# Kernel optimization log

Measured on AMD Instinct MI355X. Metric: run time of the kernel, lower is better.

## Reference

```python
import jax, jax.numpy as jnp
import numpy as np

TOP_K = 2


def setup_inputs() -> dict:
    key = jax.random.key(0)
    ks = jax.random.split(key, 4)
    T, E, D_IN, D_H, D_OUT = 8192, 8, 1024, 4096, 1024
    s_in = 1.0 / np.sqrt(D_IN)
    s_h = 1.0 / np.sqrt(D_H)
    return {
        "x": jax.random.normal(ks[0], (T, D_IN), dtype=jnp.float32),
        "Wg": jax.random.normal(ks[1], (D_IN, E), dtype=jnp.float32) * s_in,
        "bg": jnp.zeros((E,), dtype=jnp.float32),
        "W1": jax.random.normal(ks[2], (E, D_IN, D_H), dtype=jnp.float32) * s_in,
        "b1": jnp.zeros((E, D_H), dtype=jnp.float32),
        "W2": jax.random.normal(ks[3], (E, D_H, D_OUT), dtype=jnp.float32) * s_h,
        "b2": jnp.zeros((E, D_OUT), dtype=jnp.float32),
    }


def moe_forward(x, Wg, bg, W1, b1, W2, b2):
    # Top-k gate: logits [T,E] -> top-k -> softmax over the k selected logits,
    # scattered back into a dense [T,E] weight matrix (zeros elsewhere).
    logits = x @ Wg + bg                              # [T, E]
    topv, topi = jax.lax.top_k(logits, TOP_K)         # [T, k]
    topw = jax.nn.softmax(topv, axis=-1)              # [T, k]
    T, E = logits.shape
    weights = jnp.zeros((T, E), dtype=logits.dtype)
    rows = jnp.arange(T)[:, None]
    weights = weights.at[rows, topi].set(topw)        # dense gate weights [T, E]

    # Dense all-expert MLP (faithful to the naive torch module):
    h = jax.nn.relu(jnp.einsum("ti,eih->teh", x, W1) + b1[None])   # [T, E, H]
    expert_out = jnp.einsum("teh,eho->teo", h, W2) + b2[None]      # [T, E, O]

    # Top-k weighted sum over experts.
    return jnp.einsum("te,teo->to", weights, expert_out)           # [T, O]


def reference(x, Wg, bg, W1, b1, W2, b2):
    return moe_forward(x, Wg, bg, W1, b1, W2, b2)
```

## Files before the change

kernel.cpp:

```cpp
#include <hip/hip_runtime.h>
#include <hip/hip_bf16.h>
#include <stdint.h>

#define NTOK 8192
#define NE 8
#define DIN 1024
#define DH 4096
#define DOUT 1024
#define MAXMB 135

typedef __bf16 bf16;
typedef __bf16 bf16_8 __attribute__((ext_vector_type(8)));
typedef __bf16 bf16_4 __attribute__((ext_vector_type(4)));
typedef float f32_4 __attribute__((ext_vector_type(4)));

__device__ __forceinline__ void gl_lds16(const void* g, void* l) {
  __builtin_amdgcn_global_load_lds(
      (const __attribute__((address_space(1))) unsigned int*)g,
      (__attribute__((address_space(3))) unsigned int*)l, 16, 0, 0);
}

__global__ void gate_kernel(const float* __restrict__ x, const float* __restrict__ Wg,
                            const float* __restrict__ bg,
                            int* __restrict__ topi, float* __restrict__ topw) {
  int t = blockIdx.x * 4 + (threadIdx.x >> 6);
  int lane = threadIdx.x & 63;
  float acc[NE];
#pragma unroll
  for (int e = 0; e < NE; e++) acc[e] = 0.f;
  const float* xr = x + (size_t)t * DIN;
#pragma unroll
  for (int i = 0; i < DIN / 64; i++) {
    float xv = xr[lane + 64 * i];
    const float4* wr = (const float4*)(Wg + (size_t)(lane + 64 * i) * NE);
    float4 w0 = wr[0], w1 = wr[1];
    acc[0] += xv * w0.x; acc[1] += xv * w0.y; acc[2] += xv * w0.z; acc[3] += xv * w0.w;
    acc[4] += xv * w1.x; acc[5] += xv * w1.y; acc[6] += xv * w1.z; acc[7] += xv * w1.w;
  }
#pragma unroll
  for (int off = 32; off > 0; off >>= 1)
#pragma unroll
    for (int e = 0; e < NE; e++) acc[e] += __shfl_xor(acc[e], off, 64);
  if (lane == 0) {
    float lg[NE];
#pragma unroll
    for (int e = 0; e < NE; e++) lg[e] = acc[e] + bg[e];
    int i0 = 0; float v0 = lg[0];
#pragma unroll
    for (int e = 1; e < NE; e++) if (lg[e] > v0) { v0 = lg[e]; i0 = e; }
    int i1 = -1; float v1 = -3.0e38f;
#pragma unroll
    for (int e = 0; e < NE; e++) if (e != i0 && lg[e] > v1) { v1 = lg[e]; i1 = e; }
    float ex = expf(v1 - v0);
    float w0 = 1.f / (1.f + ex);
    float w1 = ex / (1.f + ex);
    topi[2 * t] = i0; topi[2 * t + 1] = i1;
    topw[2 * t] = w0; topw[2 * t + 1] = w1;
  }
}

__global__ void hist_kernel(const int* __restrict__ topi, int* __restrict__ counts,
                            int* __restrict__ pos) {
  __shared__ int bins[NE];
  __shared__ int base[NE];
  int tid = threadIdx.x;
  if (tid < NE) bins[tid] = 0;
  __syncthreads();
  int i = blockIdx.x * 256 + tid;
  int e = topi[i];
  int local = atomicAdd(&bins[e], 1);
  __syncthreads();
  if (tid < NE) base[tid] = atomicAdd(&counts[tid], bins[tid]);
  __syncthreads();
  pos[i] = base[e] + local;
}

__global__ void scan_kernel(const int* counts, int* offsets, int* mblk_off) {
  if (threadIdx.x == 0) {
    int s = 0, b = 0;
    for (int e = 0; e < NE; e++) {
      offsets[e] = s; mblk_off[e] = b;
      s += counts[e]; b += (counts[e] + 127) >> 7;
    }
    mblk_off[NE] = b;
  }
}

__global__ void pack_kernel(const int* __restrict__ topi,
                            const int* __restrict__ pos, const int* __restrict__ offsets,
                            int* __restrict__ tok_list, int* __restrict__ slot_of) {
  int i = blockIdx.x * 256 + threadIdx.x;
  int e = topi[i];
  int slot = offsets[e] + pos[i];
  tok_list[slot] = i >> 1;
  slot_of[i] = slot;
}

__global__ void cvtx_kernel(const float* __restrict__ x, bf16* __restrict__ xb) {
  size_t i = ((size_t)blockIdx.x * 256 + threadIdx.x) * 8;
  float4 a = *(const float4*)(x + i);
  float4 b = *(const float4*)(x + i + 4);
  bf16_8 o;
  o[0] = (bf16)a.x; o[1] = (bf16)a.y; o[2] = (bf16)a.z; o[3] = (bf16)a.w;
  o[4] = (bf16)b.x; o[5] = (bf16)b.y; o[6] = (bf16)b.z; o[7] = (bf16)b.w;
  *(bf16_8*)(xb + i) = o;
}

__global__ void tcvt_kernel(const float* __restrict__ src, bf16* __restrict__ dst,
                            int src_ld, long long src_es, int dst_ld, long long dst_es) {
  __shared__ bf16 tile[32][33];
  const float* s = src + blockIdx.z * src_es + (size_t)(blockIdx.x * 32) * src_ld + blockIdx.y * 32;
  bf16* d = dst + blockIdx.z * dst_es + (size_t)(blockIdx.y * 32) * dst_ld + blockIdx.x * 32;
  int tid = threadIdx.x;
  int r = tid >> 3, c4 = (tid & 7) * 4;
  float4 v = *(const float4*)(s + (size_t)r * src_ld + c4);
  tile[r][c4] = (bf16)v.x; tile[r][c4 + 1] = (bf16)v.y;
  tile[r][c4 + 2] = (bf16)v.z; tile[r][c4 + 3] = (bf16)v.w;
  __syncthreads();
  int n = tid >> 3, k4 = (tid & 7) * 4;
  bf16_4 o;
  o[0] = tile[k4][n]; o[1] = tile[k4 + 1][n]; o[2] = tile[k4 + 2][n]; o[3] = tile[k4 + 3][n];
  *(bf16_4*)(d + (size_t)n * dst_ld + k4) = o;
}


__global__ __launch_bounds__(256) void gemm1_kernel(
    const bf16* __restrict__ xb, const bf16* __restrict__ W1t,
    const float* __restrict__ b1, const int* __restrict__ counts,
    const int* __restrict__ offsets, const int* __restrict__ mblk_off,
    const int* __restrict__ tok_list,
    bf16* __restrict__ h, int hchunk, int hc0) {
  int mb = blockIdx.y;
  if (mb >= mblk_off[NE]) return;
  int e = 0;
  while (mb >= mblk_off[e + 1]) e++;
  int ne = counts[e];
  int m0 = (mb - mblk_off[e]) * 128;
  int off = offsets[e];
  int n0 = blockIdx.x * 128;

  __shared__ bf16 ldsA[128 * 32];
  __shared__ bf16 ldsB[128 * 32];

  int tid = threadIdx.x;
  int w = tid >> 6, lane = tid & 63;
  int scol = (((lane & 3) ^ (lane >> 3)) & 3) * 8;

  const bf16* gA[2]; const bf16* gB[2];
  bf16* lA[2]; bf16* lB[2];
#pragma unroll
  for (int j = 0; j < 2; j++) {
    int seg = w * 2 + j;
    int row = seg * 16 + (lane >> 2);
    int slot = off + m0 + row;
    int smax = off + ne - 1;
    if (slot > smax) slot = smax;
    int tok = tok_list[slot];
    gA[j] = xb + (size_t)tok * DIN + scol;
    lA[j] = ldsA + seg * 512;
    gB[j] = W1t + ((size_t)e * hchunk + n0 + row) * DIN + scol;
    lB[j] = ldsB + seg * 512;
  }

  f32_4 acc[4][4];
#pragma unroll
  for (int i = 0; i < 4; i++)
#pragma unroll
    for (int j = 0; j < 4; j++) acc[i][j] = (f32_4){0.f, 0.f, 0.f, 0.f};

  int wm = w & 1, wn = w >> 1;
  int lr = lane & 15, quad = lane >> 4;
  int rcol = ((quad ^ (lr >> 1)) & 3) * 8;

  for (int kt = 0; kt < DIN / 32; kt++) {
#pragma unroll
    for (int j = 0; j < 2; j++) {
      gl_lds16(gA[j], lA[j]);
      gl_lds16(gB[j], lB[j]);
    }
    gA[0] += 32; gA[1] += 32; gB[0] += 32; gB[1] += 32;
    __syncthreads();
    bf16_8 af[4], bfr[4];
#pragma unroll
    for (int mt = 0; mt < 4; mt++)
      af[mt] = *(const bf16_8*)(ldsA + (wm * 64 + mt * 16 + lr) * 32 + rcol);
#pragma unroll
    for (int nt = 0; nt < 4; nt++)
      bfr[nt] = *(const bf16_8*)(ldsB + (wn * 64 + nt * 16 + lr) * 32 + rcol);
#pragma unroll
    for (int mt = 0; mt < 4; mt++)
#pragma unroll
      for (int nt = 0; nt < 4; nt++)
        acc[mt][nt] = __builtin_amdgcn_mfma_f32_16x16x32_bf16(af[mt], bfr[nt], acc[mt][nt], 0, 0, 0);
    __syncthreads();
  }

#pragma unroll
  for (int nt = 0; nt < 4; nt++) {
    int cloc = wn * 64 + nt * 16 + lr;
    int c = n0 + cloc;
    float bias = b1[(size_t)e * DH + hc0 + c];
#pragma unroll
    for (int mt = 0; mt < 4; mt++) {
#pragma unroll
      for (int r2 = 0; r2 < 4; r2++) {
        int row = wm * 64 + mt * 16 + quad * 4 + r2;
        if (m0 + row < ne) {
          float v = acc[mt][nt][r2] + bias;
          v = v > 0.f ? v : 0.f;
          h[(size_t)(off + m0 + row) * hchunk + c] = (bf16)v;
        }
      }
    }
  }
}

__global__ __launch_bounds__(256) void gemm2_kernel(
    const bf16* __restrict__ h, const bf16* __restrict__ W2t,
    const int* __restrict__ counts, const int* __restrict__ offsets,
    const int* __restrict__ mblk_off,
    float* __restrict__ y, int hchunk, int accum) {
  int mb = blockIdx.y;
  if (mb >= mblk_off[NE]) return;
  int e = 0;
  while (mb >= mblk_off[e + 1]) e++;
  int ne = counts[e];
  int m0 = (mb - mblk_off[e]) * 128;
  int off = offsets[e];
  int n0 = blockIdx.x * 128;

  __shared__ bf16 ldsA[128 * 32];
  __shared__ bf16 ldsB[128 * 32];

  int tid = threadIdx.x;
  int w = tid >> 6, lane = tid & 63;
  int scol = (((lane & 3) ^ (lane >> 3)) & 3) * 8;

  const bf16* gA[2]; const bf16* gB[2];
  bf16* lA[2]; bf16* lB[2];
#pragma unroll
  for (int j = 0; j < 2; j++) {
    int seg = w * 2 + j;
    int row = seg * 16 + (lane >> 2);
    gA[j] = h + (size_t)(off + m0 + row) * hchunk + scol;
    lA[j] = ldsA + seg * 512;
    gB[j] = W2t + ((size_t)e * DOUT + n0 + row) * hchunk + scol;
    lB[j] = ldsB + seg * 512;
  }

  f32_4 acc[4][4];
#pragma unroll
  for (int i = 0; i < 4; i++)
#pragma unroll
    for (int j = 0; j < 4; j++) acc[i][j] = (f32_4){0.f, 0.f, 0.f, 0.f};

  int wm = w & 1, wn = w >> 1;
  int lr = lane & 15, quad = lane >> 4;
  int rcol = ((quad ^ (lr >> 1)) & 3) * 8;

  for (int kt = 0; kt < hchunk / 32; kt++) {
#pragma unroll
    for (int j = 0; j < 2; j++) {
      gl_lds16(gA[j], lA[j]);
      gl_lds16(gB[j], lB[j]);
    }
    gA[0] += 32; gA[1] += 32; gB[0] += 32; gB[1] += 32;
    __syncthreads();
    bf16_8 af[4], bfr[4];
#pragma unroll
    for (int mt = 0; mt < 4; mt++)
      af[mt] = *(const bf16_8*)(ldsA + (wm * 64 + mt * 16 + lr) * 32 + rcol);
#pragma unroll
    for (int nt = 0; nt < 4; nt++)
      bfr[nt] = *(const bf16_8*)(ldsB + (wn * 64 + nt * 16 + lr) * 32 + rcol);
#pragma unroll
    for (int mt = 0; mt < 4; mt++)
#pragma unroll
      for (int nt = 0; nt < 4; nt++)
        acc[mt][nt] = __builtin_amdgcn_mfma_f32_16x16x32_bf16(af[mt], bfr[nt], acc[mt][nt], 0, 0, 0);
    __syncthreads();
  }

#pragma unroll
  for (int mt = 0; mt < 4; mt++) {
#pragma unroll
    for (int r2 = 0; r2 < 4; r2++) {
      int row = wm * 64 + mt * 16 + quad * 4 + r2;
      if (m0 + row < ne) {
        float* yrow = y + (size_t)(off + m0 + row) * DOUT + n0;
#pragma unroll
        for (int nt = 0; nt < 4; nt++) {
          int c = wn * 64 + nt * 16 + lr;
          float v = acc[mt][nt][r2];
          if (accum) v += yrow[c];
          yrow[c] = v;
        }
      }
    }
  }
}

__global__ void combine_kernel(const int* __restrict__ topi, const float* __restrict__ topw,
                               const int* __restrict__ slot_of, const float* __restrict__ y,
                               const float* __restrict__ b2, float* __restrict__ out) {
  int t = blockIdx.x;
  int c = threadIdx.x * 4;
  int e0 = topi[2 * t], e1 = topi[2 * t + 1];
  float w0 = topw[2 * t], w1 = topw[2 * t + 1];
  int s0 = slot_of[2 * t], s1 = slot_of[2 * t + 1];
  float4 a = *(const float4*)(y + (size_t)s0 * DOUT + c);
  float4 b = *(const float4*)(y + (size_t)s1 * DOUT + c);
  float4 p = *(const float4*)(b2 + (size_t)e0 * DOUT + c);
  float4 q = *(const float4*)(b2 + (size_t)e1 * DOUT + c);
  float4 o;
  o.x = w0 * (a.x + p.x) + w1 * (b.x + q.x);
  o.y = w0 * (a.y + p.y) + w1 * (b.y + q.y);
  o.z = w0 * (a.z + p.z) + w1 * (b.z + q.z);
  o.w = w0 * (a.w + p.w) + w1 * (b.w + q.w);
  *(float4*)(out + (size_t)t * DOUT + c) = o;
}

extern "C" void kernel_launch(void* const* d_in, const int* in_sizes, int n_in,
                              void* d_out, int out_size, void* d_ws, size_t ws_size,
                              hipStream_t stream) {
  const float* x  = (const float*)d_in[0];
  const float* Wg = (const float*)d_in[1];
  const float* bg = (const float*)d_in[2];
  const float* W1 = (const float*)d_in[3];
  const float* b1 = (const float*)d_in[4];
  const float* W2 = (const float*)d_in[5];
  const float* b2 = (const float*)d_in[6];
  float* out = (float*)d_out;

  char* p = (char*)d_ws;
  int*   counts   = (int*)p;   p += 256;
  int*   offsets  = (int*)p;   p += 256;
  int*   mblk_off = (int*)p;   p += 256;
  int*   topi     = (int*)p;   p += 16384 * 4;
  float* topw     = (float*)p; p += 16384 * 4;
  int*   pos      = (int*)p;   p += 16384 * 4;
  int*   tok_list = (int*)p;   p += 16384 * 4;
  int*   slot_of  = (int*)p;   p += 16384 * 4;
  bf16*  xb       = (bf16*)p;  p += (size_t)NTOK * DIN * 2;
  float* y        = (float*)p; p += (size_t)16384 * DOUT * 4;

  size_t fixedBytes = (size_t)(p - (char*)d_ws);
  int hchunk = 4096;
  while (hchunk > 128 && fixedBytes + (size_t)hchunk * 65792 > ws_size) hchunk >>= 1;

  bf16* W1t  = (bf16*)p; p += (size_t)NE * hchunk * DIN * 2;
  bf16* W2t  = (bf16*)p; p += (size_t)NE * DOUT * hchunk * 2;
  bf16* hbuf = (bf16*)p; p += (size_t)(16384 + 128) * hchunk * 2;

  hipMemsetAsync(counts, 0, 32, stream);
  gate_kernel<<<NTOK / 4, 256, 0, stream>>>(x, Wg, bg, topi, topw);
  cvtx_kernel<<<(NTOK * DIN) / (8 * 256), 256, 0, stream>>>(x, xb);
  hist_kernel<<<64, 256, 0, stream>>>(topi, counts, pos);
  scan_kernel<<<1, 64, 0, stream>>>(counts, offsets, mblk_off);
  pack_kernel<<<64, 256, 0, stream>>>(topi, pos, offsets, tok_list, slot_of);

  int nchunks = DH / hchunk;
  for (int c = 0; c < nchunks; c++) {
    int hc0 = c * hchunk;
    tcvt_kernel<<<dim3(DIN / 32, hchunk / 32, NE), 256, 0, stream>>>(
        W1 + hc0, W1t, DH, (long long)DIN * DH, DIN, (long long)hchunk * DIN);
    tcvt_kernel<<<dim3(hchunk / 32, DOUT / 32, NE), 256, 0, stream>>>(
        W2 + (size_t)hc0 * DOUT, W2t, DOUT, (long long)DH * DOUT, hchunk, (long long)DOUT * hchunk);
    gemm1_kernel<<<dim3(hchunk / 128, MAXMB), 256, 0, stream>>>(
        xb, W1t, b1, counts, offsets, mblk_off, tok_list, hbuf, hchunk, hc0);
    gemm2_kernel<<<dim3(DOUT / 128, MAXMB), 256, 0, stream>>>(
        hbuf, W2t, counts, offsets, mblk_off, y, hchunk, c > 0 ? 1 : 0);
  }
  combine_kernel<<<NTOK, 256, 0, stream>>>(topi, topw, slot_of, y, b2, out);
}
```

Baseline: 890.1 us.

## Triple-buffer LDS loads in expert GEMMs and swizzle blocks across XCDs

Result: faster. 833.2 us (-6.4%).

```diff
diff --git a/kernel.cpp b/kernel.cpp
--- a/kernel.cpp
+++ b/kernel.cpp
@@ -124,23 +124,32 @@
 }
 
 
+
+#define XCD_SWIZZLE()                                                     \
+  int nbx = gridDim.x;                                                    \
+  int orig = blockIdx.y * nbx + blockIdx.x;                               \
+  int nwg = nbx * gridDim.y;             \
+  int wgid = (orig & 7) * (nwg >> 3) + (orig >> 3);                       \
+  int bxi = wgid % nbx;                                                   \
+  int mb = wgid / nbx;
+
 __global__ __launch_bounds__(256) void gemm1_kernel(
     const bf16* __restrict__ xb, const bf16* __restrict__ W1t,
     const float* __restrict__ b1, const int* __restrict__ counts,
     const int* __restrict__ offsets, const int* __restrict__ mblk_off,
     const int* __restrict__ tok_list,
     bf16* __restrict__ h, int hchunk, int hc0) {
-  int mb = blockIdx.y;
+  XCD_SWIZZLE();
   if (mb >= mblk_off[NE]) return;
   int e = 0;
   while (mb >= mblk_off[e + 1]) e++;
   int ne = counts[e];
   int m0 = (mb - mblk_off[e]) * 128;
   int off = offsets[e];
-  int n0 = blockIdx.x * 128;
-
-  __shared__ bf16 ldsA[128 * 32];
-  __shared__ bf16 ldsB[128 * 32];
+  int n0 = bxi * 128;
+
+  __shared__ bf16 ldsA[3 * 128 * 32];
+  __shared__ bf16 ldsB[3 * 128 * 32];
 
   int tid = threadIdx.x;
   int w = tid >> 6, lane = tid & 63;
@@ -172,27 +181,45 @@
   int lr = lane & 15, quad = lane >> 4;
   int rcol = ((quad ^ (lr >> 1)) & 3) * 8;
 
-  for (int kt = 0; kt < DIN / 32; kt++) {
-#pragma unroll
-    for (int j = 0; j < 2; j++) {
-      gl_lds16(gA[j], lA[j]);
-      gl_lds16(gB[j], lB[j]);
-    }
-    gA[0] += 32; gA[1] += 32; gB[0] += 32; gB[1] += 32;
-    __syncthreads();
+  auto compute = [&](int buf) {
     bf16_8 af[4], bfr[4];
 #pragma unroll
     for (int mt = 0; mt < 4; mt++)
-      af[mt] = *(const bf16_8*)(ldsA + (wm * 64 + mt * 16 + lr) * 32 + rcol);
+      af[mt] = *(const bf16_8*)(ldsA + buf * 4096 + (wm * 64 + mt * 16 + lr) * 32 + rcol);
 #pragma unroll
     for (int nt = 0; nt < 4; nt++)
-      bfr[nt] = *(const bf16_8*)(ldsB + (wn * 64 + nt * 16 + lr) * 32 + rcol);
+      bfr[nt] = *(const bf16_8*)(ldsB + buf * 4096 + (wn * 64 + nt * 16 + lr) * 32 + rcol);
 #pragma unroll
     for (int mt = 0; mt < 4; mt++)
 #pragma unroll
       for (int nt = 0; nt < 4; nt++)
         acc[mt][nt] = __builtin_amdgcn_mfma_f32_16x16x32_bf16(af[mt], bfr[nt], acc[mt][nt], 0, 0, 0);
-    __syncthreads();
+  };
+
+  const int nk = DIN / 32;
+#pragma unroll
+  for (int j = 0; j < 2; j++) { gl_lds16(gA[j], lA[j]); gl_lds16(gB[j], lB[j]); }
+  gA[0] += 32; gA[1] += 32; gB[0] += 32; gB[1] += 32;
+#pragma unroll
+  for (int j = 0; j < 2; j++) { gl_lds16(gA[j], lA[j] + 4096); gl_lds16(gB[j], lB[j] + 4096); }
+  gA[0] += 32; gA[1] += 32; gB[0] += 32; gB[1] += 32;
+
+  int rb = 0, sb = 2;
+  for (int kt = 0; kt < nk; kt++) {
+    if (kt + 1 < nk) asm volatile("s_waitcnt vmcnt(4)" ::: "memory");
+    else             asm volatile("s_waitcnt vmcnt(0)" ::: "memory");
+    __builtin_amdgcn_s_barrier();
+    compute(rb);
+    if (kt + 2 < nk) {
+#pragma unroll
+      for (int j = 0; j < 2; j++) {
+        gl_lds16(gA[j], lA[j] + sb * 4096);
+        gl_lds16(gB[j], lB[j] + sb * 4096);
+      }
+      gA[0] += 32; gA[1] += 32; gB[0] += 32; gB[1] += 32;
+    }
+    rb = rb == 2 ? 0 : rb + 1;
+    sb = sb == 2 ? 0 : sb + 1;
   }
 
 #pragma unroll
@@ -220,17 +247,17 @@
     const int* __restrict__ counts, const int* __restrict__ offsets,
     const int* __restrict__ mblk_off,
     float* __restrict__ y, int hchunk, int accum) {
-  int mb = blockIdx.y;
+  XCD_SWIZZLE();
   if (mb >= mblk_off[NE]) return;
   int e = 0;
   while (mb >= mblk_off[e + 1]) e++;
   int ne = counts[e];
   int m0 = (mb - mblk_off[e]) * 128;
   int off = offsets[e];
-  int n0 = blockIdx.x * 128;
-
-  __shared__ bf16 ldsA[128 * 32];
-  __shared__ bf16 ldsB[128 * 32];
+  int n0 = bxi * 128;
+
+  __shared__ bf16 ldsA[3 * 128 * 32];
+  __shared__ bf16 ldsB[3 * 128 * 32];
 
   int tid = threadIdx.x;
   int w = tid >> 6, lane = tid & 63;
@@ -258,27 +285,45 @@
   int lr = lane & 15, quad = lane >> 4;
   int rcol = ((quad ^ (lr >> 1)) & 3) * 8;
 
-  for (int kt = 0; kt < hchunk / 32; kt++) {
-#pragma unroll
-    for (int j = 0; j < 2; j++) {
-      gl_lds16(gA[j], lA[j]);
-      gl_lds16(gB[j], lB[j]);
-    }
-    gA[0] += 32; gA[1] += 32; gB[0] += 32; gB[1] += 32;
-    __syncthreads();
+  auto compute = [&](int buf) {
     bf16_8 af[4], bfr[4];
 #pragma unroll
     for (int mt = 0; mt < 4; mt++)
-      af[mt] = *(const bf16_8*)(ldsA + (wm * 64 + mt * 16 + lr) * 32 + rcol);
+      af[mt] = *(const bf16_8*)(ldsA + buf * 4096 + (wm * 64 + mt * 16 + lr) * 32 + rcol);
 #pragma unroll
     for (int nt = 0; nt < 4; nt++)
-      bfr[nt] = *(const bf16_8*)(ldsB + (wn * 64 + nt * 16 + lr) * 32 + rcol);
+      bfr[nt] = *(const bf16_8*)(ldsB + buf * 4096 + (wn * 64 + nt * 16 + lr) * 32 + rcol);
 #pragma unroll
     for (int mt = 0; mt < 4; mt++)
 #pragma unroll
       for (int nt = 0; nt < 4; nt++)
         acc[mt][nt] = __builtin_amdgcn_mfma_f32_16x16x32_bf16(af[mt], bfr[nt], acc[mt][nt], 0, 0, 0);
-    __syncthreads();
+  };
+
+  const int nk = hchunk / 32;
+#pragma unroll
+  for (int j = 0; j < 2; j++) { gl_lds16(gA[j], lA[j]); gl_lds16(gB[j], lB[j]); }
+  gA[0] += 32; gA[1] += 32; gB[0] += 32; gB[1] += 32;
+#pragma unroll
+  for (int j = 0; j < 2; j++) { gl_lds16(gA[j], lA[j] + 4096); gl_lds16(gB[j], lB[j] + 4096); }
+  gA[0] += 32; gA[1] += 32; gB[0] += 32; gB[1] += 32;
+
+  int rb = 0, sb = 2;
+  for (int kt = 0; kt < nk; kt++) {
+    if (kt + 1 < nk) asm volatile("s_waitcnt vmcnt(4)" ::: "memory");
+    else             asm volatile("s_waitcnt vmcnt(0)" ::: "memory");
+    __builtin_amdgcn_s_barrier();
+    compute(rb);
+    if (kt + 2 < nk) {
+#pragma unroll
+      for (int j = 0; j < 2; j++) {
+        gl_lds16(gA[j], lA[j] + sb * 4096);
+        gl_lds16(gB[j], lB[j] + sb * 4096);
+      }
+      gA[0] += 32; gA[1] += 32; gB[0] += 32; gB[1] += 32;
+    }
+    rb = rb == 2 ? 0 : rb + 1;
+    sb = sb == 2 ? 0 : sb + 1;
   }
 
 #pragma unroll
```

## Rewrite expert GEMMs with 256x256 tiles, double-buffered LDS, XCD swizzle, split-K

Applied to the files above, without the earlier changes.

New measurement: 807.2 us. -9.3%, faster.

```diff
diff --git a/kernel.cpp b/kernel.cpp
--- a/kernel.cpp
+++ b/kernel.cpp
@@ -7,7 +7,7 @@
 #define DIN 1024
 #define DH 4096
 #define DOUT 1024
-#define MAXMB 135
+#define MAXMB2 71
 
 typedef __bf16 bf16;
 typedef __bf16 bf16_8 __attribute__((ext_vector_type(8)));
@@ -18,6 +18,12 @@
   __builtin_amdgcn_global_load_lds(
       (const __attribute__((address_space(1))) unsigned int*)g,
       (__attribute__((address_space(3))) unsigned int*)l, 16, 0, 0);
+}
+
+__device__ __forceinline__ int xcd_swz(int orig, int nwg) {
+  int q = nwg >> 3, r = nwg & 7;
+  int x = orig & 7, i = orig >> 3;
+  return (x < r ? x * (q + 1) : r * (q + 1) + (x - r) * q) + i;
 }
 
 __global__ void gate_kernel(const float* __restrict__ x, const float* __restrict__ Wg,
@@ -80,7 +86,7 @@
     int s = 0, b = 0;
     for (int e = 0; e < NE; e++) {
       offsets[e] = s; mblk_off[e] = b;
-      s += counts[e]; b += (counts[e] + 127) >> 7;
+      s += counts[e]; b += (counts[e] + 255) >> 8;
     }
     mblk_off[NE] = b;
   }
@@ -124,177 +130,344 @@
 }
 
 
-__global__ __launch_bounds__(256) void gemm1_kernel(
+#define MFMA_ARGS 0, 0, 0
+
+__global__ __launch_bounds__(512, 2) void gemm1_kernel(
     const bf16* __restrict__ xb, const bf16* __restrict__ W1t,
     const float* __restrict__ b1, const int* __restrict__ counts,
     const int* __restrict__ offsets, const int* __restrict__ mblk_off,
     const int* __restrict__ tok_list,
     bf16* __restrict__ h, int hchunk, int hc0) {
-  int mb = blockIdx.y;
+  extern __shared__ __align__(16) bf16 smem[];
+  int gx = gridDim.x;
+  int nwg = gx * gridDim.y;
+  int orig = blockIdx.y * gx + blockIdx.x;
+  int wgid = xcd_swz(orig, nwg);
+  int bx = wgid % gx;
+  int mb = wgid / gx;
   if (mb >= mblk_off[NE]) return;
   int e = 0;
   while (mb >= mblk_off[e + 1]) e++;
   int ne = counts[e];
-  int m0 = (mb - mblk_off[e]) * 128;
+  int m0 = (mb - mblk_off[e]) * 256;
   int off = offsets[e];
-  int n0 = blockIdx.x * 128;
-
-  __shared__ bf16 ldsA[128 * 32];
-  __shared__ bf16 ldsB[128 * 32];
-
-  int tid = threadIdx.x;
-  int w = tid >> 6, lane = tid & 63;
-  int scol = (((lane & 3) ^ (lane >> 3)) & 3) * 8;
-
-  const bf16* gA[2]; const bf16* gB[2];
-  bf16* lA[2]; bf16* lB[2];
-#pragma unroll
-  for (int j = 0; j < 2; j++) {
-    int seg = w * 2 + j;
-    int row = seg * 16 + (lane >> 2);
-    int slot = off + m0 + row;
-    int smax = off + ne - 1;
-    if (slot > smax) slot = smax;
-    int tok = tok_list[slot];
-    gA[j] = xb + (size_t)tok * DIN + scol;
-    lA[j] = ldsA + seg * 512;
-    gB[j] = W1t + ((size_t)e * hchunk + n0 + row) * DIN + scol;
-    lB[j] = ldsB + seg * 512;
-  }
-
-  f32_4 acc[4][4];
-#pragma unroll
-  for (int i = 0; i < 4; i++)
+  int n0 = bx * 256;
+
+  int t = threadIdx.x;
+  int w = t >> 6, lane = t & 63;
+  int wm = w >> 2, wn = w & 3;
+  int lr = lane & 15, qd = lane >> 4;
+  int cx0 = (qd ^ (lr & 7)) << 3;
+  int cx1 = ((4 + qd) ^ (lr & 7)) << 3;
+
+  int r0 = t >> 3;
+  int cA = ((t & 7) ^ (r0 & 7)) << 3;
+  const bf16* gA[4]; const bf16* gB[4];
+#pragma unroll
+  for (int j = 0; j < 4; j++) {
+    int r = r0 + j * 64;
+    int slot = off + m0 + r;
+    int mx = off + ne - 1;
+    if (slot > mx) slot = mx;
+    gA[j] = xb + (size_t)tok_list[slot] * DIN + cA;
+    gB[j] = W1t + ((size_t)e * hchunk + n0 + r) * DIN + cA;
+  }
+
+  auto stageA = [&](int nb) {
+    bf16* db = smem + nb * 16384 + w * 512;
+    gl_lds16(gA[0], db); gl_lds16(gA[1], db + 4096);
+    gl_lds16(gA[2], db + 8192); gl_lds16(gA[3], db + 12288);
+  };
+  auto stageB = [&](int nb) {
+    bf16* db = smem + 32768 + nb * 16384 + w * 512;
+    gl_lds16(gB[0], db); gl_lds16(gB[1], db + 4096);
+    gl_lds16(gB[2], db + 8192); gl_lds16(gB[3], db + 12288);
+  };
+
+  f32_4 acc[8][4];
+#pragma unroll
+  for (int i = 0; i < 8; i++)
 #pragma unroll
     for (int j = 0; j < 4; j++) acc[i][j] = (f32_4){0.f, 0.f, 0.f, 0.f};
 
-  int wm = w & 1, wn = w >> 1;
-  int lr = lane & 15, quad = lane >> 4;
-  int rcol = ((quad ^ (lr >> 1)) & 3) * 8;
-
-  for (int kt = 0; kt < DIN / 32; kt++) {
-#pragma unroll
-    for (int j = 0; j < 2; j++) {
-      gl_lds16(gA[j], lA[j]);
-      gl_lds16(gB[j], lB[j]);
-    }
-    gA[0] += 32; gA[1] += 32; gB[0] += 32; gB[1] += 32;
-    __syncthreads();
-    bf16_8 af[4], bfr[4];
-#pragma unroll
-    for (int mt = 0; mt < 4; mt++)
-      af[mt] = *(const bf16_8*)(ldsA + (wm * 64 + mt * 16 + lr) * 32 + rcol);
-#pragma unroll
-    for (int nt = 0; nt < 4; nt++)
-      bfr[nt] = *(const bf16_8*)(ldsB + (wn * 64 + nt * 16 + lr) * 32 + rcol);
-#pragma unroll
-    for (int mt = 0; mt < 4; mt++)
-#pragma unroll
-      for (int nt = 0; nt < 4; nt++)
-        acc[mt][nt] = __builtin_amdgcn_mfma_f32_16x16x32_bf16(af[mt], bfr[nt], acc[mt][nt], 0, 0, 0);
-    __syncthreads();
+  const int nk = DIN / 64;
+  stageA(0); stageB(0);
+#pragma unroll
+  for (int j = 0; j < 4; j++) { gA[j] += 64; gB[j] += 64; }
+
+#pragma unroll 1
+  for (int kt = 0; kt < nk; kt++) {
+    asm volatile("s_waitcnt vmcnt(0)" ::: "memory");
+    __builtin_amdgcn_s_barrier();
+    __builtin_amdgcn_sched_barrier(0);
+    int cb = kt & 1, nb = cb ^ 1;
+    const bf16* pa = smem + cb * 16384 + (wm * 128 + lr) * 64;
+    const bf16* pb = smem + 32768 + cb * 16384 + (wn * 64 + lr) * 64;
+    bool pf = (kt + 1 < nk);
+    bf16_8 a_[4], fb0[4], fb1[4];
+    if (pf) stageA(nb);
+    __builtin_amdgcn_sched_barrier(0);
+#pragma unroll
+    for (int i = 0; i < 4; i++) {
+      fb0[i] = *(const bf16_8*)(pb + i * 1024 + cx0);
+      a_[i] = *(const bf16_8*)(pa + i * 1024 + cx0);
+    }
+    __builtin_amdgcn_sched_barrier(0);
+    __builtin_amdgcn_s_barrier();
+    asm volatile("s_waitcnt lgkmcnt(0)" ::: "memory");
+    __builtin_amdgcn_sched_barrier(0);
+    __builtin_amdgcn_s_setprio(1);
+#pragma unroll
+    for (int m2 = 0; m2 < 4; m2++)
+#pragma unroll
+      for (int n2 = 0; n2 < 4; n2++)
+        acc[m2][n2] = __builtin_amdgcn_mfma_f32_16x16x32_bf16(a_[m2], fb0[n2], acc[m2][n2], MFMA_ARGS);
+    __builtin_amdgcn_s_setprio(0);
+    __builtin_amdgcn_sched_barrier(0);
+    __builtin_amdgcn_s_barrier();
+    if (pf) stageB(nb);
+    __builtin_amdgcn_sched_barrier(0);
+#pragma unroll
+    for (int i = 0; i < 4; i++) a_[i] = *(const bf16_8*)(pa + (4 + i) * 1024 + cx0);
+    __builtin_amdgcn_sched_barrier(0);
+    __builtin_amdgcn_s_barrier();
+    asm volatile("s_waitcnt lgkmcnt(0)" ::: "memory");
+    __builtin_amdgcn_sched_barrier(0);
+    __builtin_amdgcn_s_setprio(1);
+#pragma unroll
+    for (int m2 = 0; m2 < 4; m2++)
+#pragma unroll
+      for (int n2 = 0; n2 < 4; n2++)
+        acc[4 + m2][n2] = __builtin_amdgcn_mfma_f32_16x16x32_bf16(a_[m2], fb0[n2], acc[4 + m2][n2], MFMA_ARGS);
+    __builtin_amdgcn_s_setprio(0);
+    __builtin_amdgcn_sched_barrier(0);
+    __builtin_amdgcn_s_barrier();
+#pragma unroll
+    for (int i = 0; i < 4; i++) {
+      fb1[i] = *(const bf16_8*)(pb + i * 1024 + cx1);
+      a_[i] = *(const bf16_8*)(pa + i * 1024 + cx1);
+    }
+    __builtin_amdgcn_sched_barrier(0);
+    __builtin_amdgcn_s_barrier();
+    asm volatile("s_waitcnt lgkmcnt(0)" ::: "memory");
+    __builtin_amdgcn_sched_barrier(0);
+    __builtin_amdgcn_s_setprio(1);
+#pragma unroll
+    for (int m2 = 0; m2 < 4; m2++)
+#pragma unroll
+      for (int n2 = 0; n2 < 4; n2++)
+        acc[m2][n2] = __builtin_amdgcn_mfma_f32_16x16x32_bf16(a_[m2], fb1[n2], acc[m2][n2], MFMA_ARGS);
+    __builtin_amdgcn_s_setprio(0);
+    __builtin_amdgcn_sched_barrier(0);
+    __builtin_amdgcn_s_barrier();
+#pragma unroll
+    for (int i = 0; i < 4; i++) a_[i] = *(const bf16_8*)(pa + (4 + i) * 1024 + cx1);
+    __builtin_amdgcn_sched_barrier(0);
+    __builtin_amdgcn_s_barrier();
+    asm volatile("s_waitcnt lgkmcnt(0)" ::: "memory");
+    __builtin_amdgcn_sched_barrier(0);
+    __builtin_amdgcn_s_setprio(1);
+#pragma unroll
+    for (int m2 = 0; m2 < 4; m2++)
+#pragma unroll
+      for (int n2 = 0; n2 < 4; n2++)
+        acc[4 + m2][n2] = __builtin_amdgcn_mfma_f32_16x16x32_bf16(a_[m2], fb1[n2], acc[4 + m2][n2], MFMA_ARGS);
+    __builtin_amdgcn_s_setprio(0);
+    __builtin_amdgcn_sched_barrier(0);
+    __builtin_amdgcn_s_barrier();
+    if (pf) {
+#pragma unroll
+      for (int j = 0; j < 4; j++) { gA[j] += 64; gB[j] += 64; }
+    }
   }
 
 #pragma unroll
   for (int nt = 0; nt < 4; nt++) {
-    int cloc = wn * 64 + nt * 16 + lr;
-    int c = n0 + cloc;
-    float bias = b1[(size_t)e * DH + hc0 + c];
-#pragma unroll
-    for (int mt = 0; mt < 4; mt++) {
+    int col = wn * 64 + nt * 16 + lr;
+    float bias = b1[(size_t)e * DH + hc0 + n0 + col];
+#pragma unroll
+    for (int mt = 0; mt < 8; mt++) {
 #pragma unroll
       for (int r2 = 0; r2 < 4; r2++) {
-        int row = wm * 64 + mt * 16 + quad * 4 + r2;
-        if (m0 + row < ne) {
-          float v = acc[mt][nt][r2] + bias;
-          v = v > 0.f ? v : 0.f;
-          h[(size_t)(off + m0 + row) * hchunk + c] = (bf16)v;
-        }
+        int row = wm * 128 + mt * 16 + qd * 4 + r2;
+        float v = acc[mt][nt][r2] + bias;
+        v = v > 0.f ? v : 0.f;
+        int byte = ((row << 9) + (col << 1)) ^ (((row >> 2) & 3) << 5);
+        *(bf16*)((char*)smem + byte) = (bf16)v;
       }
     }
   }
-}
-
-__global__ __launch_bounds__(256) void gemm2_kernel(
+  __syncthreads();
+#pragma unroll
+  for (int p = 0; p < 16; p++) {
+    int row = p * 16 + (t >> 5);
+    int cc = t & 31;
+    if (m0 + row < ne) {
+      int byte = (((row << 9) + (cc << 4))) ^ (((row >> 2) & 3) << 5);
+      bf16_8 v = *(const bf16_8*)((char*)smem + byte);
+      *(bf16_8*)(h + (size_t)(off + m0 + row) * hchunk + n0 + cc * 8) = v;
+    }
+  }
+}
+
+__global__ __launch_bounds__(512, 2) void gemm2_kernel(
     const bf16* __restrict__ h, const bf16* __restrict__ W2t,
     const int* __restrict__ counts, const int* __restrict__ offsets,
     const int* __restrict__ mblk_off,
-    float* __restrict__ y, int hchunk, int accum) {
-  int mb = blockIdx.y;
+    float* __restrict__ y, int hchunk) {
+  extern __shared__ __align__(16) bf16 smem[];
+  int gx = gridDim.x, gy = gridDim.y;
+  int nwg = gx * gy * gridDim.z;
+  int orig = (blockIdx.z * gy + blockIdx.y) * gx + blockIdx.x;
+  int wgid = xcd_swz(orig, nwg);
+  int bx = wgid % gx;
+  int rest = wgid / gx;
+  int mb = rest % gy;
+  int z = rest / gy;
   if (mb >= mblk_off[NE]) return;
   int e = 0;
   while (mb >= mblk_off[e + 1]) e++;
   int ne = counts[e];
-  int m0 = (mb - mblk_off[e]) * 128;
+  int m0 = (mb - mblk_off[e]) * 256;
   int off = offsets[e];
-  int n0 = blockIdx.x * 128;
-
-  __shared__ bf16 ldsA[128 * 32];
-  __shared__ bf16 ldsB[128 * 32];
-
-  int tid = threadIdx.x;
-  int w = tid >> 6, lane = tid & 63;
-  int scol = (((lane & 3) ^ (lane >> 3)) & 3) * 8;
-
-  const bf16* gA[2]; const bf16* gB[2];
-  bf16* lA[2]; bf16* lB[2];
-#pragma unroll
-  for (int j = 0; j < 2; j++) {
-    int seg = w * 2 + j;
-    int row = seg * 16 + (lane >> 2);
-    gA[j] = h + (size_t)(off + m0 + row) * hchunk + scol;
-    lA[j] = ldsA + seg * 512;
-    gB[j] = W2t + ((size_t)e * DOUT + n0 + row) * hchunk + scol;
-    lB[j] = ldsB + seg * 512;
-  }
-
-  f32_4 acc[4][4];
-#pragma unroll
-  for (int i = 0; i < 4; i++)
+  int n0 = bx * 256;
+  int k0 = z * (hchunk >> 1);
+
+  int t = threadIdx.x;
+  int w = t >> 6, lane = t & 63;
+  int wm = w >> 2, wn = w & 3;
+  int lr = lane & 15, qd = lane >> 4;
+  int cx0 = (qd ^ (lr & 7)) << 3;
+  int cx1 = ((4 + qd) ^ (lr & 7)) << 3;
+
+  int r0 = t >> 3;
+  int cA = ((t & 7) ^ (r0 & 7)) << 3;
+  const bf16* gA[4]; const bf16* gB[4];
+#pragma unroll
+  for (int j = 0; j < 4; j++) {
+    int r = r0 + j * 64;
+    gA[j] = h + (size_t)(off + m0 + r) * hchunk + k0 + cA;
+    gB[j] = W2t + ((size_t)e * DOUT + n0 + r) * hchunk + k0 + cA;
+  }
+
+  auto stageA = [&](int nb) {
+    bf16* db = smem + nb * 16384 + w * 512;
+    gl_lds16(gA[0], db); gl_lds16(gA[1], db + 4096);
+    gl_lds16(gA[2], db + 8192); gl_lds16(gA[3], db + 12288);
+  };
+  auto stageB = [&](int nb) {
+    bf16* db = smem + 32768 + nb * 16384 + w * 512;
+    gl_lds16(gB[0], db); gl_lds16(gB[1], db + 4096);
+    gl_lds16(gB[2], db + 8192); gl_lds16(gB[3], db + 12288);
+  };
+
+  f32_4 acc[8][4];
+#pragma unroll
+  for (int i = 0; i < 8; i++)
 #pragma unroll
     for (int j = 0; j < 4; j++) acc[i][j] = (f32_4){0.f, 0.f, 0.f, 0.f};
 
-  int wm = w & 1, wn = w >> 1;
-  int lr = lane & 15, quad = lane >> 4;
-  int rcol = ((quad ^ (lr >> 1)) & 3) * 8;
-
-  for (int kt = 0; kt < hchunk / 32; kt++) {
-#pragma unroll
-    for (int j = 0; j < 2; j++) {
-      gl_lds16(gA[j], lA[j]);
-      gl_lds16(gB[j], lB[j]);
-    }
-    gA[0] += 32; gA[1] += 32; gB[0] += 32; gB[1] += 32;
-    __syncthreads();
-    bf16_8 af[4], bfr[4];
-#pragma unroll
-    for (int mt = 0; mt < 4; mt++)
-      af[mt] = *(const bf16_8*)(ldsA + (wm * 64 + mt * 16 + lr) * 32 + rcol);
-#pragma unroll
-    for (int nt = 0; nt < 4; nt++)
-      bfr[nt] = *(const bf16_8*)(ldsB + (wn * 64 + nt * 16 + lr) * 32 + rcol);
-#pragma unroll
-    for (int mt = 0; mt < 4; mt++)
-#pragma unroll
-      for (int nt = 0; nt < 4; nt++)
-        acc[mt][nt] = __builtin_amdgcn_mfma_f32_16x16x32_bf16(af[mt], bfr[nt], acc[mt][nt], 0, 0, 0);
-    __syncthreads();
-  }
-
-#pragma unroll
-  for (int mt = 0; mt < 4; mt++) {
+  const int nk = hchunk >> 7;
+  stageA(0); stageB(0);
+#pragma unroll
+  for (int j = 0; j < 4; j++) { gA[j] += 64; gB[j] += 64; }
+
+#pragma unroll 1
+  for (int kt = 0; kt < nk; kt++) {
+    asm volatile("s_waitcnt vmcnt(0)" ::: "memory");
+    __builtin_amdgcn_s_barrier();
+    __builtin_amdgcn_sched_barrier(0);
+    int cb = kt & 1, nb = cb ^ 1;
+    const bf16* pa = smem + cb * 16384 + (wm * 128 + lr) * 64;
+    const bf16* pb = smem + 32768 + cb * 16384 + (wn * 64 + lr) * 64;
+    bool pf = (kt + 1 < nk);
+    bf16_8 a_[4], fb0[4], fb1[4];
+    if (pf) stageA(nb);
+    __builtin_amdgcn_sched_barrier(0);
+#pragma unroll
+    for (int i = 0; i < 4; i++) {
+      fb0[i] = *(const bf16_8*)(pb + i * 1024 + cx0);
+      a_[i] = *(const bf16_8*)(pa + i * 1024 + cx0);
+    }
+    __builtin_amdgcn_sched_barrier(0);
+    __builtin_amdgcn_s_barrier();
+    asm volatile("s_waitcnt lgkmcnt(0)" ::: "memory");
+    __builtin_amdgcn_sched_barrier(0);
+    __builtin_amdgcn_s_setprio(1);
+#pragma unroll
+    for (int m2 = 0; m2 < 4; m2++)
+#pragma unroll
+      for (int n2 = 0; n2 < 4; n2++)
+        acc[m2][n2] = __builtin_amdgcn_mfma_f32_16x16x32_bf16(a_[m2], fb0[n2], acc[m2][n2], MFMA_ARGS);
+    __builtin_amdgcn_s_setprio(0);
+    __builtin_amdgcn_sched_barrier(0);
+    __builtin_amdgcn_s_barrier();
+    if (pf) stageB(nb);
+    __builtin_amdgcn_sched_barrier(0);
+#pragma unroll
+    for (int i = 0; i < 4; i++) a_[i] = *(const bf16_8*)(pa + (4 + i) * 1024 + cx0);
+    __builtin_amdgcn_sched_barrier(0);
+    __builtin_amdgcn_s_barrier();
+    asm volatile("s_waitcnt lgkmcnt(0)" ::: "memory");
+    __builtin_amdgcn_sched_barrier(0);
+    __builtin_amdgcn_s_setprio(1);
+#pragma unroll
+    for (int m2 = 0; m2 < 4; m2++)
+#pragma unroll
+      for (int n2 = 0; n2 < 4; n2++)
+        acc[4 + m2][n2] = __builtin_amdgcn_mfma_f32_16x16x32_bf16(a_[m2], fb0[n2], acc[4 + m2][n2], MFMA_ARGS);
+    __builtin_amdgcn_s_setprio(0);
+    __builtin_amdgcn_sched_barrier(0);
+    __builtin_amdgcn_s_barrier();
+#pragma unroll
+    for (int i = 0; i < 4; i++) {
+      fb1[i] = *(const bf16_8*)(pb + i * 1024 + cx1);
+      a_[i] = *(const bf16_8*)(pa + i * 1024 + cx1);
+    }
+    __builtin_amdgcn_sched_barrier(0);
+    __builtin_amdgcn_s_barrier();
+    asm volatile("s_waitcnt lgkmcnt(0)" ::: "memory");
+    __builtin_amdgcn_sched_barrier(0);
+    __builtin_amdgcn_s_setprio(1);
+#pragma unroll
+    for (int m2 = 0; m2 < 4; m2++)
+#pragma unroll
+      for (int n2 = 0; n2 < 4; n2++)
+        acc[m2][n2] = __builtin_amdgcn_mfma_f32_16x16x32_bf16(a_[m2], fb1[n2], acc[m2][n2], MFMA_ARGS);
+    __builtin_amdgcn_s_setprio(0);
+    __builtin_amdgcn_sched_barrier(0);
+    __builtin_amdgcn_s_barrier();
+#pragma unroll
+    for (int i = 0; i < 4; i++) a_[i] = *(const bf16_8*)(pa + (4 + i) * 1024 + cx1);
+    __builtin_amdgcn_sched_barrier(0);
+    __builtin_amdgcn_s_barrier();
+    asm volatile("s_waitcnt lgkmcnt(0)" ::: "memory");
+    __builtin_amdgcn_sched_barrier(0);
+    __builtin_amdgcn_s_setprio(1);
+#pragma unroll
+    for (int m2 = 0; m2 < 4; m2++)
+#pragma unroll
+      for (int n2 = 0; n2 < 4; n2++)
+        acc[4 + m2][n2] = __builtin_amdgcn_mfma_f32_16x16x32_bf16(a_[m2], fb1[n2], acc[4 + m2][n2], MFMA_ARGS);
+    __builtin_amdgcn_s_setprio(0);
+    __builtin_amdgcn_sched_barrier(0);
+    __builtin_amdgcn_s_barrier();
+    if (pf) {
+#pragma unroll
+      for (int j = 0; j < 4; j++) { gA[j] += 64; gB[j] += 64; }
+    }
+  }
+
+#pragma unroll
+  for (int mt = 0; mt < 8; mt++) {
 #pragma unroll
     for (int r2 = 0; r2 < 4; r2++) {
-      int row = wm * 64 + mt * 16 + quad * 4 + r2;
+      int row = wm * 128 + mt * 16 + qd * 4 + r2;
       if (m0 + row < ne) {
-        float* yrow = y + (size_t)(off + m0 + row) * DOUT + n0;
-#pragma unroll
-        for (int nt = 0; nt < 4; nt++) {
-          int c = wn * 64 + nt * 16 + lr;
-          float v = acc[mt][nt][r2];
-          if (accum) v += yrow[c];
-          yrow[c] = v;
-        }
+        float* yr = y + (size_t)(off + m0 + row) * DOUT + n0;
+#pragma unroll
+        for (int nt = 0; nt < 4; nt++)
+          atomicAdd(yr + wn * 64 + nt * 16 + lr, acc[mt][nt][r2]);
       }
     }
   }
@@ -332,6 +505,15 @@
   const float* b2 = (const float*)d_in[6];
   float* out = (float*)d_out;
 
+  static bool attrset = false;
+  if (!attrset) {
+    hipFuncSetAttribute((const void*)gemm1_kernel,
+                        hipFuncAttributeMaxDynamicSharedMemorySize, 131072);
+    hipFuncSetAttribute((const void*)gemm2_kernel,
+                        hipFuncAttributeMaxDynamicSharedMemorySize, 131072);
+    attrset = true;
+  }
+
   char* p = (char*)d_ws;
   int*   counts   = (int*)p;   p += 256;
   int*   offsets  = (int*)p;   p += 256;
@@ -346,13 +528,14 @@
 
   size_t fixedBytes = (size_t)(p - (char*)d_ws);
   int hchunk = 4096;
-  while (hchunk > 128 && fixedBytes + (size_t)hchunk * 65792 > ws_size) hchunk >>= 1;
+  while (hchunk > 256 && fixedBytes + (size_t)hchunk * 66048 > ws_size) hchunk >>= 1;
 
   bf16* W1t  = (bf16*)p; p += (size_t)NE * hchunk * DIN * 2;
   bf16* W2t  = (bf16*)p; p += (size_t)NE * DOUT * hchunk * 2;
-  bf16* hbuf = (bf16*)p; p += (size_t)(16384 + 128) * hchunk * 2;
+  bf16* hbuf = (bf16*)p; p += (size_t)(16384 + 256) * hchunk * 2;
 
   hipMemsetAsync(counts, 0, 32, stream);
+  hipMemsetAsync(y, 0, (size_t)16384 * DOUT * 4, stream);
   gate_kernel<<<NTOK / 4, 256, 0, stream>>>(x, Wg, bg, topi, topw);
   cvtx_kernel<<<(NTOK * DIN) / (8 * 256), 256, 0, stream>>>(x, xb);
   hist_kernel<<<64, 256, 0, stream>>>(topi, counts, pos);
@@ -366,10 +549,10 @@
         W1 + hc0, W1t, DH, (long long)DIN * DH, DIN, (long long)hchunk * DIN);
     tcvt_kernel<<<dim3(hchunk / 32, DOUT / 32, NE), 256, 0, stream>>>(
         W2 + (size_t)hc0 * DOUT, W2t, DOUT, (long long)DH * DOUT, hchunk, (long long)DOUT * hchunk);
-    gemm1_kernel<<<dim3(hchunk / 128, MAXMB), 256, 0, stream>>>(
+    gemm1_kernel<<<dim3(hchunk / 256, MAXMB2), 512, 131072, stream>>>(
         xb, W1t, b1, counts, offsets, mblk_off, tok_list, hbuf, hchunk, hc0);
-    gemm2_kernel<<<dim3(DOUT / 128, MAXMB), 256, 0, stream>>>(
-        hbuf, W2t, counts, offsets, mblk_off, y, hchunk, c > 0 ? 1 : 0);
+    gemm2_kernel<<<dim3(DOUT / 256, MAXMB2, 2), 512, 131072, stream>>>(
+        hbuf, W2t, counts, offsets, mblk_off, y, hchunk);
   }
   combine_kernel<<<NTOK, 256, 0, stream>>>(topi, topw, slot_of, y, b2, out);
 }
```
